# Kernel optimization log

Measured on AMD Instinct MI355X. Metric: run time of the kernel, lower is better.

The kernel has to match this reference:

```python
import jax, jax.numpy as jnp
import numpy as np

B, NFIELD, NEMB, NFILTER, NLAYERS = 256, 64, 64, 128, 3


def setup_inputs() -> dict:
    key = jax.random.key(0)
    ks = jax.random.split(key, 5)
    x = jax.random.normal(ks[0], (B, NFIELD, NEMB), dtype=jnp.float32)
    # Conv1d(k=1, bias=False) weights, squeezed to (out_ch, in_ch). Small init for stability.
    W0 = jax.random.normal(ks[1], (NFILTER, NFIELD * NFIELD), dtype=jnp.float32) * 0.02
    W1 = jax.random.normal(ks[2], (NFILTER, NFIELD * NFILTER), dtype=jnp.float32) * 0.02
    W2 = jax.random.normal(ks[3], (NFILTER, NFIELD * NFILTER), dtype=jnp.float32) * 0.02
    Wa = jax.random.normal(ks[4], (1, NLAYERS * NFILTER), dtype=jnp.float32) * 0.02
    return {"x": x, "W0": W0, "W1": W1, "W2": W2, "Wa": Wa}


def reference(x, W0, W1, W2, Wa):
    # x: (B, F, E). CIN recurrence over a fixed small number of layers.
    Ws = [W0, W1, W2]
    x0 = x
    xk = x
    pooled = []
    for W in Ws:
        # outer product over field axes: (B, F, C, E)
        h = x0[:, :, None, :] * xk[:, None, :, :]
        b, f, c, e = h.shape
        h = h.reshape(b, f * c, e)
        # 1x1 conv == GEMM over channel dim, then ReLU
        xk = jax.nn.relu(jnp.einsum('oc,bce->boe', W, h))
        # sum-pool over embedding dim: (B, nfilter)
        pooled.append(jnp.sum(xk, axis=-1))
    feats = jnp.concatenate(pooled, axis=1)  # (B, nlayers*nfilter)
    y = feats @ Wa.T                         # (B, 1)
    return y[:, 0]
```

## Files before the change

### kernel.cpp

```cpp
#include <hip/hip_runtime.h>

#define NBATCH 256
#define NFILT  128

typedef __attribute__((ext_vector_type(8))) short bf16x8;
typedef __attribute__((ext_vector_type(4))) float f32x4;

__device__ __forceinline__ unsigned short f2b(float f) {
    unsigned u = __float_as_uint(f);
    u = (u + 0x7fffu + ((u >> 16) & 1u)) >> 16;
    return (unsigned short)u;
}
__device__ __forceinline__ float b2f(unsigned short h) {
    return __uint_as_float(((unsigned)h) << 16);
}
__device__ __forceinline__ void async16(const void* g, void* l) {
    __builtin_amdgcn_global_load_lds((const __attribute__((address_space(1))) unsigned int*)g,
                                     (__attribute__((address_space(3))) unsigned int*)l, 16, 0, 0);
}

__global__ void prep_all(const float* __restrict__ x,
                         const float* __restrict__ W0,
                         const float* __restrict__ W1,
                         const float* __restrict__ W2,
                         unsigned short* __restrict__ x0t,
                         unsigned short* __restrict__ x0f,
                         unsigned short* __restrict__ Wp0,
                         unsigned short* __restrict__ Wp1,
                         unsigned short* __restrict__ Wp2)
{
    const int bid = blockIdx.x, tid = threadIdx.x;
    if (bid < 10240) {
        const float* W; unsigned short* Wp; int CLOG, KLOG, idx;
        if (bid < 2048)      { W = W0; Wp = Wp0; CLOG = 6; KLOG = 12; idx = bid * 256 + tid; }
        else if (bid < 6144) { W = W1; Wp = Wp1; CLOG = 7; KLOG = 13; idx = (bid - 2048) * 256 + tid; }
        else                 { W = W2; Wp = Wp2; CLOG = 7; KLOG = 13; idx = (bid - 6144) * 256 + tid; }
        int o = idx >> KLOG, k = idx & ((1 << KLOG) - 1);
        int f = k >> CLOG, c = k & ((1 << CLOG) - 1);
        int rg = o >> 4, l15 = o & 15;
        int cs = c >> 5, kseg = (c >> 3) & 3, j = c & 7;
        int NCS = 1 << (CLOG - 5);
        int NK = 64 * NCS;
        int kstep = f * NCS + cs;
        size_t dst = (((size_t)rg * NK + kstep) * 64 + kseg * 16 + l15) * 8 + j;
        Wp[dst] = f2b(W[idx]);
    } else {
        int idx = (bid - 10240) * 256 + tid;
        int b = idx >> 12, r = idx & 4095, f = r >> 6, e = r & 63;
        unsigned short v = f2b(x[idx]);
        x0f[b * 4096 + f * 64 + e] = v;
        x0t[b * 4096 + e * 64 + f] = v;
    }
}

template <int CL, bool LAST>
__global__ __launch_bounds__(512) void layer_k(
    const unsigned short* __restrict__ Wp,
    const unsigned short* __restrict__ Bsrc,
    const unsigned short* __restrict__ x0f,
    const float* __restrict__ Wa_l,
    unsigned short* __restrict__ xknext,
    float* __restrict__ ybuf)
{
    constexpr int NCS = CL / 32;
    constexpr int NK  = 64 * NCS;
    constexpr int NG  = NK / 4;
    extern __shared__ char sm[];
    const int bid = blockIdx.x, tid = threadIdx.x;
    const int rg = bid & 7, sg = bid >> 3;
    const int lane = tid & 63, w = tid >> 6;
    const int l15 = lane & 15, kseg = lane >> 4;
    const int b = sg * 8 + w;

    {
        const char* src = (const char*)x0f + (size_t)b * 8192 + lane * 16;
        char* dst = sm + w * 8192;
#pragma unroll
        for (int i = 0; i < 8; ++i) async16(src + i * 1024, dst + i * 1024);
    }

    bf16x8 bq[NCS][4];
    const char* Bb = (const char*)Bsrc + (size_t)b * (CL * 128) + kseg * 16;
#pragma unroll
    for (int cs = 0; cs < NCS; ++cs)
#pragma unroll
        for (int nt = 0; nt < 4; ++nt)
            bq[cs][nt] = *(const bf16x8*)(Bb + (nt * 16 + l15) * (CL * 2) + cs * 64);

    const char* Ag = (const char*)Wp + ((size_t)rg * NK) * 1024 + (kseg * 16 + l15) * 16;
    bf16x8 aq[4];
    aq[0] = *(const bf16x8*)(Ag);
    aq[1] = *(const bf16x8*)(Ag + 1024);

    __syncthreads();

    const unsigned short* XF = (const unsigned short*)(sm + w * 8192);
    const f32x4 ZERO = {0.f, 0.f, 0.f, 0.f};
    f32x4 acc[4], accf[4];
#pragma unroll
    for (int nt = 0; nt < 4; ++nt) acc[nt] = ZERO;

    for (int g = 0; g < NG; ++g) {
        const size_t k0 = (size_t)g * 4;
        float sA[4], sB[4];
        if (NCS == 4) {
#pragma unroll
            for (int nt = 0; nt < 4; ++nt) sA[nt] = b2f(XF[g * 64 + nt * 16 + l15]);
        } else {
#pragma unroll
            for (int nt = 0; nt < 4; ++nt) {
                sA[nt] = b2f(XF[(2 * g) * 64 + nt * 16 + l15]);
                sB[nt] = b2f(XF[(2 * g + 1) * 64 + nt * 16 + l15]);
            }
        }
        aq[2] = *(const bf16x8*)(Ag + (k0 + 2) * 1024);
#pragma unroll
        for (int nt = 0; nt < 4; ++nt)
            accf[nt] = __builtin_amdgcn_mfma_f32_16x16x32_bf16(aq[0], bq[0][nt], ZERO, 0, 0, 0);
        aq[3] = *(const bf16x8*)(Ag + (k0 + 3) * 1024);
#pragma unroll
        for (int nt = 0; nt < 4; ++nt)
            accf[nt] = __builtin_amdgcn_mfma_f32_16x16x32_bf16(aq[1], bq[1 & (NCS - 1)][nt], accf[nt], 0, 0, 0);
        if (NCS == 2) {
#pragma unroll
            for (int nt = 0; nt < 4; ++nt) {
                const f32x4 sv = {sA[nt], sA[nt], sA[nt], sA[nt]};
                acc[nt] += accf[nt] * sv;
            }
        }
        aq[0] = *(const bf16x8*)(Ag + (k0 + 4) * 1024);
#pragma unroll
        for (int nt = 0; nt < 4; ++nt)
            accf[nt] = __builtin_amdgcn_mfma_f32_16x16x32_bf16(aq[2], bq[2 & (NCS - 1)][nt],
                                                               (NCS == 2) ? ZERO : accf[nt], 0, 0, 0);
        aq[1] = *(const bf16x8*)(Ag + (k0 + 5) * 1024);
#pragma unroll
        for (int nt = 0; nt < 4; ++nt)
            accf[nt] = __builtin_amdgcn_mfma_f32_16x16x32_bf16(aq[3], bq[3 & (NCS - 1)][nt], accf[nt], 0, 0, 0);
        {
            const float* sf = (NCS == 2) ? sB : sA;
#pragma unroll
            for (int nt = 0; nt < 4; ++nt) {
                const f32x4 sv = {sf[nt], sf[nt], sf[nt], sf[nt]};
                acc[nt] += accf[nt] * sv;
            }
        }
    }

    const float4 wa = *(const float4*)(Wa_l + rg * 16 + kseg * 4);
    float ypart = 0.f;
#pragma unroll
    for (int nt = 0; nt < 4; ++nt) {
        f32x4 v = acc[nt];
        v.x = fmaxf(v.x, 0.f); v.y = fmaxf(v.y, 0.f);
        v.z = fmaxf(v.z, 0.f); v.w = fmaxf(v.w, 0.f);
        ypart = fmaf(wa.x, v.x, ypart);
        ypart = fmaf(wa.y, v.y, ypart);
        ypart = fmaf(wa.z, v.z, ypart);
        ypart = fmaf(wa.w, v.w, ypart);
        if (!LAST) {
            unsigned lo = (unsigned)f2b(v.x) | ((unsigned)f2b(v.y) << 16);
            unsigned hi = (unsigned)f2b(v.z) | ((unsigned)f2b(v.w) << 16);
            *(uint2*)((char*)xknext + (size_t)b * 16384 + (nt * 16 + l15) * 256
                      + (rg * 16 + kseg * 4) * 2) = make_uint2(lo, hi);
        }
    }
#pragma unroll
    for (int off = 32; off >= 1; off >>= 1)
        ypart += __shfl_down(ypart, off, 64);
    if (lane == 0) ybuf[b * 8 + rg] = ypart;
}

__global__ void finalize_k(const float* __restrict__ ybuf, float* __restrict__ y) {
    const int b = threadIdx.x;
    float s = 0.f;
#pragma unroll
    for (int l = 0; l < 3; ++l)
#pragma unroll
        for (int r = 0; r < 8; ++r)
            s += ybuf[l * 2048 + b * 8 + r];
    y[b] = s;
}

extern "C" void kernel_launch(void* const* d_in, const int* in_sizes, int n_in,
                              void* d_out, int out_size, void* d_ws, size_t ws_size,
                              hipStream_t stream) {
    const float* x  = (const float*)d_in[0];
    const float* W0 = (const float*)d_in[1];
    const float* W1 = (const float*)d_in[2];
    const float* W2 = (const float*)d_in[3];
    const float* Wa = (const float*)d_in[4];
    float* y = (float*)d_out;

    char* ws = (char*)d_ws;
    unsigned short* Wp0  = (unsigned short*)(ws + 0x000000);
    unsigned short* Wp1  = (unsigned short*)(ws + 0x110000);
    unsigned short* Wp2  = (unsigned short*)(ws + 0x320000);
    unsigned short* x0t  = (unsigned short*)(ws + 0x530000);
    unsigned short* x0f  = (unsigned short*)(ws + 0x730000);
    unsigned short* xkA  = (unsigned short*)(ws + 0x930000);
    unsigned short* xkB  = (unsigned short*)(ws + 0xD30000);
    float*          ybuf = (float*)(ws + 0x1130000);

    hipLaunchKernelGGL(prep_all, dim3(14336), dim3(256), 0, stream,
                       x, W0, W1, W2, x0t, x0f, Wp0, Wp1, Wp2);

    hipFuncSetAttribute((const void*)layer_k<64, false>,
                        hipFuncAttributeMaxDynamicSharedMemorySize, 65536);
    hipFuncSetAttribute((const void*)layer_k<128, false>,
                        hipFuncAttributeMaxDynamicSharedMemorySize, 65536);
    hipFuncSetAttribute((const void*)layer_k<128, true>,
                        hipFuncAttributeMaxDynamicSharedMemorySize, 65536);

    hipLaunchKernelGGL((layer_k<64, false>), dim3(256), dim3(512), 65536, stream,
                       Wp0, x0t, x0f, Wa + 0, xkA, ybuf + 0);
    hipLaunchKernelGGL((layer_k<128, false>), dim3(256), dim3(512), 65536, stream,
                       Wp1, xkA, x0f, Wa + 128, xkB, ybuf + 2048);
    hipLaunchKernelGGL((layer_k<128, true>), dim3(256), dim3(512), 65536, stream,
                       Wp2, xkB, x0f, Wa + 256, xkA, ybuf + 4096);

    hipLaunchKernelGGL(finalize_k, dim3(1), dim3(256), 0, stream, ybuf, y);
}
```

Measured before the change: 118.9 us.

## Stage shared weight tiles in LDS with double-buffered async loads; vectorize prep

In the layer kernels, all 8 waves of a block use the same weight rows. The A operand was previously loaded by each wave from global memory on its own. Now the block cooperatively stages 16KB weight chunks into LDS with async global-to-LDS copies, double-buffered across chunks with a barrier per chunk, so each wave reads A from LDS and redundant global/L2 traffic goes away. The prep kernel now converts four elements per thread with float4 loads and ushort4 stores. The change raises LDS use to 96KB and adds per-chunk block synchronisation.

```diff
diff --git a/kernel.cpp b/kernel.cpp
--- a/kernel.cpp
+++ b/kernel.cpp
@@ -1,7 +1,6 @@
 #include <hip/hip_runtime.h>
 
 #define NBATCH 256
-#define NFILT  128
 
 typedef __attribute__((ext_vector_type(8))) short bf16x8;
 typedef __attribute__((ext_vector_type(4))) float f32x4;
@@ -30,12 +29,13 @@
                          unsigned short* __restrict__ Wp2)
 {
     const int bid = blockIdx.x, tid = threadIdx.x;
-    if (bid < 10240) {
-        const float* W; unsigned short* Wp; int CLOG, KLOG, idx;
-        if (bid < 2048)      { W = W0; Wp = Wp0; CLOG = 6; KLOG = 12; idx = bid * 256 + tid; }
-        else if (bid < 6144) { W = W1; Wp = Wp1; CLOG = 7; KLOG = 13; idx = (bid - 2048) * 256 + tid; }
-        else                 { W = W2; Wp = Wp2; CLOG = 7; KLOG = 13; idx = (bid - 6144) * 256 + tid; }
-        int o = idx >> KLOG, k = idx & ((1 << KLOG) - 1);
+    if (bid < 2560) {
+        const float* W; unsigned short* Wp; int CLOG, KLOG, lbid;
+        if (bid < 512)       { W = W0; Wp = Wp0; CLOG = 6; KLOG = 12; lbid = bid; }
+        else if (bid < 1536) { W = W1; Wp = Wp1; CLOG = 7; KLOG = 13; lbid = bid - 512; }
+        else                 { W = W2; Wp = Wp2; CLOG = 7; KLOG = 13; lbid = bid - 1536; }
+        const int base = (lbid * 256 + tid) * 4;
+        int o = base >> KLOG, k = base & ((1 << KLOG) - 1);
         int f = k >> CLOG, c = k & ((1 << CLOG) - 1);
         int rg = o >> 4, l15 = o & 15;
         int cs = c >> 5, kseg = (c >> 3) & 3, j = c & 7;
@@ -43,18 +43,24 @@
         int NK = 64 * NCS;
         int kstep = f * NCS + cs;
         size_t dst = (((size_t)rg * NK + kstep) * 64 + kseg * 16 + l15) * 8 + j;
-        Wp[dst] = f2b(W[idx]);
+        const float4 wv = *(const float4*)(W + base);
+        ushort4 ov = make_ushort4(f2b(wv.x), f2b(wv.y), f2b(wv.z), f2b(wv.w));
+        *(ushort4*)(Wp + dst) = ov;
     } else {
-        int idx = (bid - 10240) * 256 + tid;
-        int b = idx >> 12, r = idx & 4095, f = r >> 6, e = r & 63;
-        unsigned short v = f2b(x[idx]);
-        x0f[b * 4096 + f * 64 + e] = v;
-        x0t[b * 4096 + e * 64 + f] = v;
+        const int base = ((bid - 2560) * 256 + tid) * 4;
+        int b = base >> 12, r = base & 4095, f = r >> 6, e0 = r & 63;
+        const float4 xv = *(const float4*)(x + base);
+        ushort4 v = make_ushort4(f2b(xv.x), f2b(xv.y), f2b(xv.z), f2b(xv.w));
+        *(ushort4*)(x0f + b * 4096 + f * 64 + e0) = v;
+        x0t[b * 4096 + (e0 + 0) * 64 + f] = v.x;
+        x0t[b * 4096 + (e0 + 1) * 64 + f] = v.y;
+        x0t[b * 4096 + (e0 + 2) * 64 + f] = v.z;
+        x0t[b * 4096 + (e0 + 3) * 64 + f] = v.w;
     }
 }
 
 template <int CL, bool LAST>
-__global__ __launch_bounds__(512) void layer_k(
+__global__ __launch_bounds__(512, 1) void layer_k(
     const unsigned short* __restrict__ Wp,
     const unsigned short* __restrict__ Bsrc,
     const unsigned short* __restrict__ x0f,
@@ -64,8 +70,11 @@
 {
     constexpr int NCS = CL / 32;
     constexpr int NK  = 64 * NCS;
-    constexpr int NG  = NK / 4;
+    constexpr int NCH = NK / 16;
+    constexpr int NFOLD = 16 / NCS;
     extern __shared__ char sm[];
+    char* smA = sm;
+    char* smX = sm + 32768;
     const int bid = blockIdx.x, tid = threadIdx.x;
     const int rg = bid & 7, sg = bid >> 3;
     const int lane = tid & 63, w = tid >> 6;
@@ -74,77 +83,65 @@
 
     {
         const char* src = (const char*)x0f + (size_t)b * 8192 + lane * 16;
-        char* dst = sm + w * 8192;
+        char* dst = smX + w * 8192;
 #pragma unroll
         for (int i = 0; i < 8; ++i) async16(src + i * 1024, dst + i * 1024);
     }
 
     bf16x8 bq[NCS][4];
-    const char* Bb = (const char*)Bsrc + (size_t)b * (CL * 128) + kseg * 16;
-#pragma unroll
-    for (int cs = 0; cs < NCS; ++cs)
-#pragma unroll
-        for (int nt = 0; nt < 4; ++nt)
-            bq[cs][nt] = *(const bf16x8*)(Bb + (nt * 16 + l15) * (CL * 2) + cs * 64);
-
-    const char* Ag = (const char*)Wp + ((size_t)rg * NK) * 1024 + (kseg * 16 + l15) * 16;
-    bf16x8 aq[4];
-    aq[0] = *(const bf16x8*)(Ag);
-    aq[1] = *(const bf16x8*)(Ag + 1024);
-
+    {
+        const char* Bb = (const char*)Bsrc + (size_t)b * (CL * 128) + kseg * 16;
+#pragma unroll
+        for (int cs = 0; cs < NCS; ++cs)
+#pragma unroll
+            for (int nt = 0; nt < 4; ++nt)
+                bq[cs][nt] = *(const bf16x8*)(Bb + (nt * 16 + l15) * (CL * 2) + cs * 64);
+    }
+
+    const char* Ab = (const char*)Wp + (size_t)rg * NK * 1024;
+    auto stage = [&](int ch, int buf) {
+        const char* src = Ab + (size_t)ch * 16384 + w * 2048 + lane * 16;
+        char* dst = smA + buf * 16384 + w * 2048;
+        async16(src, dst);
+        async16(src + 1024, dst + 1024);
+    };
+    stage(0, 0);
     __syncthreads();
 
-    const unsigned short* XF = (const unsigned short*)(sm + w * 8192);
+    const unsigned short* XF = (const unsigned short*)(smX + w * 8192);
     const f32x4 ZERO = {0.f, 0.f, 0.f, 0.f};
     f32x4 acc[4], accf[4];
 #pragma unroll
     for (int nt = 0; nt < 4; ++nt) acc[nt] = ZERO;
 
-    for (int g = 0; g < NG; ++g) {
-        const size_t k0 = (size_t)g * 4;
-        float sA[4], sB[4];
-        if (NCS == 4) {
-#pragma unroll
-            for (int nt = 0; nt < 4; ++nt) sA[nt] = b2f(XF[g * 64 + nt * 16 + l15]);
-        } else {
-#pragma unroll
-            for (int nt = 0; nt < 4; ++nt) {
-                sA[nt] = b2f(XF[(2 * g) * 64 + nt * 16 + l15]);
-                sB[nt] = b2f(XF[(2 * g + 1) * 64 + nt * 16 + l15]);
+    for (int ch = 0; ch < NCH; ++ch) {
+        const int cur = ch & 1;
+        if (ch + 1 < NCH) stage(ch + 1, cur ^ 1);
+#pragma unroll
+        for (int cs = 0; cs < NCS; ++cs)
+            asm volatile("" :: "v"(bq[cs][0]), "v"(bq[cs][1]), "v"(bq[cs][2]), "v"(bq[cs][3]));
+        const char* Abuf = smA + cur * 16384 + lane * 16;
+#pragma unroll
+        for (int gi = 0; gi < NFOLD; ++gi) {
+            const int fg = ch * NFOLD + gi;
+            const float sv0 = b2f(XF[fg * 64 + l15]);
+            const float sv1 = b2f(XF[fg * 64 + 16 + l15]);
+            const float sv2 = b2f(XF[fg * 64 + 32 + l15]);
+            const float sv3 = b2f(XF[fg * 64 + 48 + l15]);
+#pragma unroll
+            for (int cs = 0; cs < NCS; ++cs) {
+                const bf16x8 a = *(const bf16x8*)(Abuf + (gi * NCS + cs) * 1024);
+#pragma unroll
+                for (int nt = 0; nt < 4; ++nt)
+                    accf[nt] = __builtin_amdgcn_mfma_f32_16x16x32_bf16(
+                        a, bq[cs][nt], (cs == 0) ? ZERO : accf[nt], 0, 0, 0);
             }
+            acc[0] += accf[0] * sv0;
+            acc[1] += accf[1] * sv1;
+            acc[2] += accf[2] * sv2;
+            acc[3] += accf[3] * sv3;
         }
-        aq[2] = *(const bf16x8*)(Ag + (k0 + 2) * 1024);
-#pragma unroll
-        for (int nt = 0; nt < 4; ++nt)
-            accf[nt] = __builtin_amdgcn_mfma_f32_16x16x32_bf16(aq[0], bq[0][nt], ZERO, 0, 0, 0);
-        aq[3] = *(const bf16x8*)(Ag + (k0 + 3) * 1024);
-#pragma unroll
-        for (int nt = 0; nt < 4; ++nt)
-            accf[nt] = __builtin_amdgcn_mfma_f32_16x16x32_bf16(aq[1], bq[1 & (NCS - 1)][nt], accf[nt], 0, 0, 0);
-        if (NCS == 2) {
-#pragma unroll
-            for (int nt = 0; nt < 4; ++nt) {
-                const f32x4 sv = {sA[nt], sA[nt], sA[nt], sA[nt]};
-                acc[nt] += accf[nt] * sv;
-            }
-        }
-        aq[0] = *(const bf16x8*)(Ag + (k0 + 4) * 1024);
-#pragma unroll
-        for (int nt = 0; nt < 4; ++nt)
-            accf[nt] = __builtin_amdgcn_mfma_f32_16x16x32_bf16(aq[2], bq[2 & (NCS - 1)][nt],
-                                                               (NCS == 2) ? ZERO : accf[nt], 0, 0, 0);
-        aq[1] = *(const bf16x8*)(Ag + (k0 + 5) * 1024);
-#pragma unroll
-        for (int nt = 0; nt < 4; ++nt)
-            accf[nt] = __builtin_amdgcn_mfma_f32_16x16x32_bf16(aq[3], bq[3 & (NCS - 1)][nt], accf[nt], 0, 0, 0);
-        {
-            const float* sf = (NCS == 2) ? sB : sA;
-#pragma unroll
-            for (int nt = 0; nt < 4; ++nt) {
-                const f32x4 sv = {sf[nt], sf[nt], sf[nt], sf[nt]};
-                acc[nt] += accf[nt] * sv;
-            }
-        }
+        __syncthreads();
     }
 
     const float4 wa = *(const float4*)(Wa_l + rg * 16 + kseg * 4);
@@ -202,21 +199,21 @@
     unsigned short* xkB  = (unsigned short*)(ws + 0xD30000);
     float*          ybuf = (float*)(ws + 0x1130000);
 
-    hipLaunchKernelGGL(prep_all, dim3(14336), dim3(256), 0, stream,
+    hipLaunchKernelGGL(prep_all, dim3(3584), dim3(256), 0, stream,
                        x, W0, W1, W2, x0t, x0f, Wp0, Wp1, Wp2);
 
     hipFuncSetAttribute((const void*)layer_k<64, false>,
-                        hipFuncAttributeMaxDynamicSharedMemorySize, 65536);
+                        hipFuncAttributeMaxDynamicSharedMemorySize, 98304);
     hipFuncSetAttribute((const void*)layer_k<128, false>,
-                        hipFuncAttributeMaxDynamicSharedMemorySize, 65536);
+                        hipFuncAttributeMaxDynamicSharedMemorySize, 98304);
     hipFuncSetAttribute((const void*)layer_k<128, true>,
-                        hipFuncAttributeMaxDynamicSharedMemorySize, 65536);
-
-    hipLaunchKernelGGL((layer_k<64, false>), dim3(256), dim3(512), 65536, stream,
+                        hipFuncAttributeMaxDynamicSharedMemorySize, 98304);
+
+    hipLaunchKernelGGL((layer_k<64, false>), dim3(256), dim3(512), 98304, stream,
                        Wp0, x0t, x0f, Wa + 0, xkA, ybuf + 0);
-    hipLaunchKernelGGL((layer_k<128, false>), dim3(256), dim3(512), 65536, stream,
+    hipLaunchKernelGGL((layer_k<128, false>), dim3(256), dim3(512), 98304, stream,
                        Wp1, xkA, x0f, Wa + 128, xkB, ybuf + 2048);
-    hipLaunchKernelGGL((layer_k<128, true>), dim3(256), dim3(512), 65536, stream,
+    hipLaunchKernelGGL((layer_k<128, true>), dim3(256), dim3(512), 98304, stream,
                        Wp2, xkB, x0f, Wa + 256, xkA, ybuf + 4096);
 
     hipLaunchKernelGGL(finalize_k, dim3(1), dim3(256), 0, stream, ybuf, y);
```

Result: faster. 100.3 us (-15.6%).
